# Kernel tuning notes

Hardware: AMD Instinct MI355X
Metric: run time of the kernel (lower is better)

## Reference

```python
import jax, jax.numpy as jnp
import numpy as np

NUM_TOKENS = 131072
INPUT_DIM = 1024
NUM_EXPERTS = 8
TOP_K = 2


def setup_inputs() -> dict:
    key = jax.random.key(0)
    kx, kw, kb = jax.random.split(key, 3)
    x = jax.random.normal(kx, (NUM_TOKENS, INPUT_DIM), dtype=jnp.float32)
    # nn.Linear(input_dim, num_experts): W [E, D], b [E]
    lim = 1.0 / np.sqrt(INPUT_DIM)
    W = jax.random.uniform(kw, (NUM_EXPERTS, INPUT_DIM), dtype=jnp.float32, minval=-lim, maxval=lim)
    b = jax.random.uniform(kb, (NUM_EXPERTS,), dtype=jnp.float32, minval=-lim, maxval=lim)
    return {"x": x, "W": W, "b": b}


def reference(x, W, b):
    # gating_scores = gate(x): [N, E]
    logits = jnp.einsum('nd,ed->ne', x, W) + b
    probs = jax.nn.softmax(logits, axis=1)
    # torch.topk returns (values, indices); module returns (indices, values)
    top_k_values, top_k_indices = jax.lax.top_k(probs, TOP_K)
    return (top_k_indices, top_k_values)
```

## Files before the change

### kernel.cpp

```cpp
#include <hip/hip_runtime.h>
#include <math.h>


#define NUM_TOKENS 131072
#define DIM        1024
#define D4         (DIM / 4)
#define NE         8
#define TPB        256
#define TOKW       64
#define DC         64
#define DC4        (DC / 4)
#define NCHUNK     (DIM / DC)
#define RS4        17

__global__ __launch_bounds__(TPB, 2)
void topk_gating_kernel(const float* __restrict__ x,
                        const float* __restrict__ W,
                        const float* __restrict__ b,
                        float* __restrict__ out)
{
    __shared__ float4 lds4[4 * TOKW * RS4];

    const int t    = threadIdx.x;
    const int wave = t >> 6;
    const int lane = t & 63;
    const int wtok0 = blockIdx.x * TPB + wave * TOKW;
    float4* wb4 = lds4 + wave * TOKW * RS4;

    const float4* x4 = (const float4*)x;
    const float4* W4 = (const float4*)W;

    const int h  = lane >> 4;
    const int lo = lane & 15;

    float acc[NE];
#pragma unroll
    for (int e = 0; e < NE; ++e) acc[e] = 0.f;

    float4 pf[16];
#pragma unroll
    for (int q = 0; q < 16; ++q) {
        int r = q * 4 + h;
        pf[q] = x4[(size_t)(wtok0 + r) * D4 + lo];
    }

    for (int c = 0; c < NCHUNK; ++c) {
#pragma unroll
        for (int q = 0; q < 16; ++q) {
            int r = q * 4 + h;
            wb4[r * RS4 + lo] = pf[q];
        }
        if (c + 1 < NCHUNK) {
#pragma unroll
            for (int q = 0; q < 16; ++q) {
                int r = q * 4 + h;
                pf[q] = x4[(size_t)(wtok0 + r) * D4 + (c + 1) * DC4 + lo];
            }
        }
#pragma unroll
        for (int j = 0; j < DC4; ++j) {
            float4 xv = wb4[lane * RS4 + j];
#pragma unroll
            for (int e = 0; e < NE; ++e) {
                float4 w = W4[e * D4 + c * DC4 + j];
                acc[e] = fmaf(xv.x, w.x, acc[e]);
                acc[e] = fmaf(xv.y, w.y, acc[e]);
                acc[e] = fmaf(xv.z, w.z, acc[e]);
                acc[e] = fmaf(xv.w, w.w, acc[e]);
            }
        }
    }

    float logit[NE];
#pragma unroll
    for (int e = 0; e < NE; ++e) logit[e] = acc[e] + b[e];

    float v1 = -INFINITY, v2 = -INFINITY;
    int   i1 = 0,         i2 = 0;
#pragma unroll
    for (int e = 0; e < NE; ++e) {
        float v = logit[e];
        if (v > v1)      { v2 = v1; i2 = i1; v1 = v; i1 = e; }
        else if (v > v2) { v2 = v;  i2 = e; }
    }

    float sum = 0.f;
#pragma unroll
    for (int e = 0; e < NE; ++e) sum += __expf(logit[e] - v1);
    float inv = 1.0f / sum;
    float p1  = inv;
    float p2  = __expf(v2 - v1) * inv;

    int n = wtok0 + lane;
    float2* outi = (float2*)out;
    float2* outv = (float2*)(out + 2 * (size_t)NUM_TOKENS);
    outi[n] = make_float2((float)i1, (float)i2);
    outv[n] = make_float2(p1, p2);
}

extern "C" void kernel_launch(void* const* d_in, const int* in_sizes, int n_in,
                              void* d_out, int out_size, void* d_ws, size_t ws_size,
                              hipStream_t stream) {
    const float* x = (const float*)d_in[0];
    const float* W = (const float*)d_in[1];
    const float* b = (const float*)d_in[2];
    float* out = (float*)d_out;

    dim3 grid(NUM_TOKENS / TPB);
    dim3 block(TPB);
    topk_gating_kernel<<<grid, block, 0, stream>>>(x, W, b, out);
}
```

Before: 903.9 us.

## Stage W in LDS, use persistent grid and split D across lanes with shuffles

Replaces the per-wave x transpose through LDS with a scheme where 16 lanes split each token's dimension and read x directly, coalesced. Partial dot products are reduced with xor shuffles. W is cached once per block in shared memory and reused across many 32-token tiles in a persistent grid-stride loop of 512 blocks. The aim is to remove the LDS staging traffic and the repeated global W reads so the kernel runs closer to the x read bandwidth. The cost is 64 accumulators per thread, which raises register pressure, plus redundant softmax work in 15 of every 16 lanes.

```diff
diff --git a/kernel.cpp b/kernel.cpp
--- a/kernel.cpp
+++ b/kernel.cpp
@@ -7,11 +7,10 @@
 #define D4         (DIM / 4)
 #define NE         8
 #define TPB        256
-#define TOKW       64
-#define DC         64
-#define DC4        (DC / 4)
-#define NCHUNK     (DIM / DC)
-#define RS4        17
+#define NBLK       512
+#define TG         8
+#define TILE_TOK   (TG * 4)
+#define NTILES     (NUM_TOKENS / TILE_TOK)
 
 __global__ __launch_bounds__(TPB, 2)
 void topk_gating_kernel(const float* __restrict__ x,
@@ -19,83 +18,84 @@
                         const float* __restrict__ b,
                         float* __restrict__ out)
 {
-    __shared__ float4 lds4[4 * TOKW * RS4];
+    __shared__ float4 Wl[NE * D4];
+    const float4* W4 = (const float4*)W;
+    for (int i = threadIdx.x; i < NE * D4; i += TPB) Wl[i] = W4[i];
+    __syncthreads();
 
-    const int t    = threadIdx.x;
-    const int wave = t >> 6;
-    const int lane = t & 63;
-    const int wtok0 = blockIdx.x * TPB + wave * TOKW;
-    float4* wb4 = lds4 + wave * TOKW * RS4;
+    const int wave = threadIdx.x >> 6;
+    const int lane = threadIdx.x & 63;
+    const int r    = lane >> 4;
+    const int lo   = lane & 15;
+    const int gw   = blockIdx.x * 4 + wave;
 
     const float4* x4 = (const float4*)x;
-    const float4* W4 = (const float4*)W;
+    float2* outi = (float2*)out;
+    float2* outv = (float2*)(out + 2 * (size_t)NUM_TOKENS);
 
-    const int h  = lane >> 4;
-    const int lo = lane & 15;
+    for (int tile = gw; tile < NTILES; tile += NBLK * 4) {
+        const int tok0 = tile * TILE_TOK;
 
-    float acc[NE];
+        float acc[TG][NE];
 #pragma unroll
-    for (int e = 0; e < NE; ++e) acc[e] = 0.f;
+        for (int g = 0; g < TG; ++g)
+#pragma unroll
+            for (int e = 0; e < NE; ++e) acc[g][e] = 0.f;
 
-    float4 pf[16];
 #pragma unroll
-    for (int q = 0; q < 16; ++q) {
-        int r = q * 4 + h;
-        pf[q] = x4[(size_t)(wtok0 + r) * D4 + lo];
-    }
+        for (int j = 0; j < 16; ++j) {
+            float4 w[NE];
+#pragma unroll
+            for (int e = 0; e < NE; ++e) w[e] = Wl[e * D4 + j * 16 + lo];
 
-    for (int c = 0; c < NCHUNK; ++c) {
 #pragma unroll
-        for (int q = 0; q < 16; ++q) {
-            int r = q * 4 + h;
-            wb4[r * RS4 + lo] = pf[q];
-        }
-        if (c + 1 < NCHUNK) {
+            for (int g = 0; g < TG; ++g) {
+                float4 xv = x4[(size_t)(tok0 + g * 4 + r) * D4 + j * 16 + lo];
 #pragma unroll
-            for (int q = 0; q < 16; ++q) {
-                int r = q * 4 + h;
-                pf[q] = x4[(size_t)(wtok0 + r) * D4 + (c + 1) * DC4 + lo];
+                for (int e = 0; e < NE; ++e) {
+                    acc[g][e] = fmaf(xv.x, w[e].x, acc[g][e]);
+                    acc[g][e] = fmaf(xv.y, w[e].y, acc[g][e]);
+                    acc[g][e] = fmaf(xv.z, w[e].z, acc[g][e]);
+                    acc[g][e] = fmaf(xv.w, w[e].w, acc[g][e]);
+                }
             }
         }
+
 #pragma unroll
-        for (int j = 0; j < DC4; ++j) {
-            float4 xv = wb4[lane * RS4 + j];
+        for (int g = 0; g < TG; ++g) {
+            float logit[NE];
 #pragma unroll
             for (int e = 0; e < NE; ++e) {
-                float4 w = W4[e * D4 + c * DC4 + j];
-                acc[e] = fmaf(xv.x, w.x, acc[e]);
-                acc[e] = fmaf(xv.y, w.y, acc[e]);
-                acc[e] = fmaf(xv.z, w.z, acc[e]);
-                acc[e] = fmaf(xv.w, w.w, acc[e]);
+                float v = acc[g][e];
+                v += __shfl_xor(v, 1);
+                v += __shfl_xor(v, 2);
+                v += __shfl_xor(v, 4);
+                v += __shfl_xor(v, 8);
+                logit[e] = v + b[e];
+            }
+
+            float v1 = -INFINITY, v2 = -INFINITY;
+            int   i1 = 0,         i2 = 0;
+#pragma unroll
+            for (int e = 0; e < NE; ++e) {
+                float v = logit[e];
+                if (v > v1)      { v2 = v1; i2 = i1; v1 = v; i1 = e; }
+                else if (v > v2) { v2 = v;  i2 = e; }
+            }
+            float sum = 0.f;
+#pragma unroll
+            for (int e = 0; e < NE; ++e) sum += __expf(logit[e] - v1);
+            float inv = 1.0f / sum;
+            float p1  = inv;
+            float p2  = __expf(v2 - v1) * inv;
+
+            if (lo == 0) {
+                int n = tok0 + g * 4 + r;
+                outi[n] = make_float2((float)i1, (float)i2);
+                outv[n] = make_float2(p1, p2);
             }
         }
     }
-
-    float logit[NE];
-#pragma unroll
-    for (int e = 0; e < NE; ++e) logit[e] = acc[e] + b[e];
-
-    float v1 = -INFINITY, v2 = -INFINITY;
-    int   i1 = 0,         i2 = 0;
-#pragma unroll
-    for (int e = 0; e < NE; ++e) {
-        float v = logit[e];
-        if (v > v1)      { v2 = v1; i2 = i1; v1 = v; i1 = e; }
-        else if (v > v2) { v2 = v;  i2 = e; }
-    }
-
-    float sum = 0.f;
-#pragma unroll
-    for (int e = 0; e < NE; ++e) sum += __expf(logit[e] - v1);
-    float inv = 1.0f / sum;
-    float p1  = inv;
-    float p2  = __expf(v2 - v1) * inv;
-
-    int n = wtok0 + lane;
-    float2* outi = (float2*)out;
-    float2* outv = (float2*)(out + 2 * (size_t)NUM_TOKENS);
-    outi[n] = make_float2((float)i1, (float)i2);
-    outv[n] = make_float2(p1, p2);
 }
 
 extern "C" void kernel_launch(void* const* d_in, const int* in_sizes, int n_in,
@@ -106,7 +106,5 @@
     const float* b = (const float*)d_in[2];
     float* out = (float*)d_out;
 
-    dim3 grid(NUM_TOKENS / TPB);
-    dim3 block(TPB);
-    topk_gating_kernel<<<grid, block, 0, stream>>>(x, W, b, out);
+    topk_gating_kernel<<<dim3(NBLK), dim3(TPB), 0, stream>>>(x, W, b, out);
 }
```

Result: slower. 1.520 ms (+68.2%).
